# Kernel optimization log

Measured on AMD Instinct MI355X. Metric: run time of the kernel, lower is better.

## Reference

```python
import jax, jax.numpy as jnp
import numpy as np

DIM = 128
N_NODES = 100000     # total semantic-network nodes per graph
N_EDGES = 800000
META0 = 20000        # output_dim0: offset of author block in graph 0
META1 = 20000        # output_dim1
AUTHOR_NUM = 50000   # args.author_num
B = 8192             # batch (chunked into B/2 pairs)
OUT_DIM = 2          # output_dim


def _linear_params(k, out_d, in_d):
    kw, kb = jax.random.split(k)
    s = 1.0 / np.sqrt(in_d)
    W = jax.random.uniform(kw, (out_d, in_d), minval=-s, maxval=s, dtype=jnp.float32)
    b = jax.random.uniform(kb, (out_d,), minval=-s, maxval=s, dtype=jnp.float32)
    return W, b


def setup_inputs() -> dict:
    key = jax.random.key(0)
    ks = jax.random.split(key, 24)
    inp = {
        'semantic_embedding0': jax.random.normal(ks[0], (N_NODES, DIM), jnp.float32),
        'interval0': jax.random.uniform(ks[1], (N_EDGES,), jnp.float32),
        'edge_index0': jax.random.randint(ks[2], (2, N_EDGES), 0, N_NODES, jnp.int64 if jax.config.jax_enable_x64 else jnp.int32),
        'semantic_embedding1': jax.random.normal(ks[3], (N_NODES, DIM), jnp.float32),
        'interval1': jax.random.uniform(ks[4], (N_EDGES,), jnp.float32),
        'edge_index1': jax.random.randint(ks[5], (2, N_EDGES), 0, N_NODES, jnp.int64 if jax.config.jax_enable_x64 else jnp.int32),
        'central_node_emb0': jax.random.normal(ks[6], (B, DIM), jnp.float32),
        'central_node_emb1': jax.random.normal(ks[7], (B, DIM), jnp.float32),
        'data': jax.random.randint(ks[8], (B,), 0, AUTHOR_NUM, jnp.int64 if jax.config.jax_enable_x64 else jnp.int32),
        'structure_embedding': jax.random.normal(ks[9], (B, DIM), jnp.float32),
    }
    inp['W1'], inp['b1'] = _linear_params(ks[10], DIM * 5, DIM)
    inp['W2'], inp['b2'] = _linear_params(ks[11], OUT_DIM, DIM * 5)
    inp['W3'], inp['b3'] = _linear_params(ks[12], DIM, DIM)
    inp['W4'], inp['b4'] = _linear_params(ks[13], DIM, DIM)
    inp['W6'], inp['b6'] = _linear_params(ks[14], DIM, DIM)
    inp['W7'], inp['b7'] = _linear_params(ks[15], DIM, DIM)
    inp['W9'], inp['b9'] = _linear_params(ks[16], DIM, DIM)
    inp['W10'], inp['b10'] = _linear_params(ks[17], DIM, DIM)
    inp['W12'], inp['b12'] = _linear_params(ks[18], DIM, DIM)
    inp['Wc'], inp['bc'] = _linear_params(ks[19], DIM, DIM * 3)
    # Hawkes decay params (nn.Parameter zeros(128,1); small random so decay is nontrivial)
    inp['hp0'] = jax.random.normal(ks[20], (DIM, 1), jnp.float32) * 0.02
    inp['hp1'] = jax.random.normal(ks[21], (DIM, 1), jnp.float32) * 0.02
    return inp


def _hawkes(interval, emb, edge_index, params, meta_size):
    # gather -> exp temporal decay -> scatter-add
    row, col = edge_index[0], edge_index[1]
    theta = (emb @ params)[col]                      # [E, 1]
    x_j = jnp.exp(interval[:, None] * theta) * emb[col]  # [E, D]
    agg = jax.ops.segment_sum(x_j, row, num_segments=N_NODES)  # [N, D]
    return agg[meta_size:meta_size + AUTHOR_NUM]     # [AUTHOR_NUM, D]


def reference(semantic_embedding0, interval0, edge_index0,
              semantic_embedding1, interval1, edge_index1,
              central_node_emb0, central_node_emb1, data, structure_embedding,
              W1, b1, W2, b2, W3, b3, W4, b4, W6, b6, W7, b7,
              W9, b9, W10, b10, W12, b12, Wc, bc, hp0, hp1):
    e0 = semantic_embedding0 @ W3.T + b3
    e1 = semantic_embedding1 @ W4.T + b4
    e0 = jax.nn.relu(_hawkes(interval0, e0, edge_index0, hp0, META0))
    e1 = jax.nn.relu(_hawkes(interval1, e1, edge_index1, hp1, META1))
    e0 = e0[data] @ W6.T + b6
    e1 = e1[data] @ W7.T + b7
    e0 = central_node_emb0 @ W9.T + b9 + e0
    e1 = central_node_emb1 @ W10.T + b10 + e1
    e3 = structure_embedding @ W12.T + b12
    cat = jnp.concatenate([e0, e1, e3], axis=1)      # [B, 3D]
    emb = jax.nn.relu(cat @ Wc.T + bc)               # Concat_Layer
    pre, suf = jnp.split(emb, 2, axis=0)
    emb = jnp.abs(pre - suf)                         # [B/2, D]
    emb = jax.nn.relu(emb @ W1.T + b1)
    # dropout is identity in eval mode
    return emb @ W2.T + b2                           # [B/2, OUT_DIM]
```

## Files before the change

kernel.cpp:

```cpp
#include <hip/hip_runtime.h>
#include <hip/hip_bf16.h>
#include <hip/hip_fp16.h>

typedef _Float16 f16;
typedef __attribute__((ext_vector_type(8))) _Float16 f16x8;
typedef __attribute__((ext_vector_type(4))) float f32x4;

#define N_NODES 100000
#define N_EDGES 800000
#define META 20000
#define AUTHORS 50000
#define BATCH 8192
#define DIM 128
#define CAP 40

__device__ __forceinline__ f16x8 cvtf8(const float* p) {
    float4 x = *(const float4*)p, y = *(const float4*)(p + 4);
    f16x8 a;
    a[0] = (f16)x.x; a[1] = (f16)x.y; a[2] = (f16)x.z; a[3] = (f16)x.w;
    a[4] = (f16)y.x; a[5] = (f16)y.y; a[6] = (f16)y.z; a[7] = (f16)y.w;
    return a;
}

__global__ __launch_bounds__(256) void k_prep_fuse(
    const float* __restrict__ Wc, const float* __restrict__ W9,
    const float* __restrict__ W6, const float* __restrict__ W10,
    const float* __restrict__ W7, const float* __restrict__ W12,
    const float* __restrict__ W3, const float* __restrict__ W4,
    const float* __restrict__ bc, const float* __restrict__ b9,
    const float* __restrict__ b6, const float* __restrict__ b10,
    const float* __restrict__ b7, const float* __restrict__ b12,
    const float* __restrict__ b3, const float* __restrict__ b4,
    const float* __restrict__ hp0, const float* __restrict__ hp1,
    const float* __restrict__ W1, const int* __restrict__ data,
    f16* __restrict__ G, float* __restrict__ biasF, f16* __restrict__ W1F,
    f16* __restrict__ W3F, f16* __restrict__ W4F, float* __restrict__ uc,
    int* __restrict__ needed, int* __restrict__ nneed)
{
    const int blk = blockIdx.x;
    const int tid = threadIdx.x;
    if (blk < 5) {
        __shared__ f16 Wt[128 * 136];
        const float* Wsrc; int co;
        switch (blk) {
            case 0: Wsrc = W9;  co = 0;   break;
            case 1: Wsrc = W6;  co = 0;   break;
            case 2: Wsrc = W10; co = 128; break;
            case 3: Wsrc = W7;  co = 128; break;
            default: Wsrc = W12; co = 256; break;
        }
#pragma unroll 4
        for (int i = 0; i < 64; ++i) {
            const int flat = i * 256 + tid;
            const int k = flat >> 7, t = flat & 127;
            Wt[t * 136 + k] = (f16)Wsrc[flat];
        }
        __syncthreads();
        const int w = tid >> 6, lane = tid & 63;
        const int quad = lane >> 4, l16 = lane & 15;
        f32x4 acc[2][8];
#pragma unroll
        for (int dt = 0; dt < 2; ++dt)
#pragma unroll
            for (int nt = 0; nt < 8; ++nt) acc[dt][nt] = (f32x4)(0.0f);
#pragma unroll
        for (int ks = 0; ks < 4; ++ks) {
            const int k0 = ks * 32 + quad * 8;
#pragma unroll
            for (int dt = 0; dt < 2; ++dt) {
                const int row = w * 32 + dt * 16 + l16;
                f16x8 a = cvtf8(Wc + row * 384 + co + k0);
#pragma unroll
                for (int nt = 0; nt < 8; ++nt) {
                    f16x8 b = *(const f16x8*)&Wt[(nt * 16 + l16) * 136 + k0];
                    acc[dt][nt] = __builtin_amdgcn_mfma_f32_16x16x32_f16(a, b, acc[dt][nt], 0, 0, 0);
                }
            }
        }
#pragma unroll
        for (int dt = 0; dt < 2; ++dt)
#pragma unroll
            for (int nt = 0; nt < 8; ++nt)
#pragma unroll
                for (int r = 0; r < 4; ++r)
                    G[(blk * 128 + w * 32 + dt * 16 + quad * 4 + r) * 128 + nt * 16 + l16] =
                        (f16)acc[dt][nt][r];
    } else if (blk == 5) {
        __shared__ float hpl[256];
        __shared__ float bsum[384];
        hpl[tid] = (tid < 128) ? hp0[tid] : hp1[tid - 128];
        for (int i = tid; i < 384; i += 256) {
            float v;
            if (i < 128) v = b9[i] + b6[i];
            else if (i < 256) v = b10[i - 128] + b7[i - 128];
            else v = b12[i - 256];
            bsum[i] = v;
        }
        __syncthreads();
        {
            const int t = tid & 127;
            const float* W = (tid < 128) ? W3 : W4;
            const float* hh = (tid < 128) ? hpl : hpl + 128;
            float s = 0.f;
#pragma unroll 8
            for (int k = 0; k < 128; ++k) s += W[k * 128 + t] * hh[k];
            uc[(tid < 128 ? 0 : 132) + t] = s;
        }
        if (tid == 0) {
            float s = 0.f;
#pragma unroll 8
            for (int k = 0; k < 128; ++k) s += b3[k] * hpl[k];
            uc[128] = s;
        }
        if (tid == 64) {
            float s = 0.f;
#pragma unroll 8
            for (int k = 0; k < 128; ++k) s += b4[k] * hpl[128 + k];
            uc[132 + 128] = s;
        }
        if (tid < 128) {
            float s = bc[tid];
#pragma unroll 8
            for (int k = 0; k < 384; ++k) s += Wc[tid * 384 + k] * bsum[k];
            biasF[tid] = s;
        }
    } else if (blk < 11) {
        const long base = (long)(blk - 6) * 2048;
#pragma unroll
        for (int i = 0; i < 8; ++i) {
            const long c = base + i * 256 + tid;
            *(f16x8*)(W1F + c * 8) = cvtf8(W1 + c * 8);
        }
    } else if (blk == 11) {
#pragma unroll
        for (int i = 0; i < 8; ++i) {
            const long c = i * 256 + tid;
            *(f16x8*)(W3F + c * 8) = cvtf8(W3 + c * 8);
        }
    } else if (blk == 12) {
#pragma unroll
        for (int i = 0; i < 8; ++i) {
            const long c = i * 256 + tid;
            *(f16x8*)(W4F + c * 8) = cvtf8(W4 + c * 8);
        }
    } else {
        const int i = (blk - 13) * 256 + tid;
        const int a = data[i];
        const int old = atomicCAS(&needed[a], 0, -1);
        if (old == 0) needed[a] = 1 + atomicAdd(nneed, 1);
    }
}

__global__ __launch_bounds__(256) void k_count_emit(
    const int* __restrict__ ei0, const float* __restrict__ iv0,
    const int* __restrict__ ei1, const float* __restrict__ iv1,
    const int* __restrict__ needed,
    int* __restrict__ count, int2* __restrict__ bucket)
{
    const int z = blockIdx.z;
    const int* rows = z ? ei1 : ei0;
    const int* cols = rows + N_EDGES;
    const float* ivp = z ? iv1 : iv0;

    const int e0 = (blockIdx.x * 256 + threadIdx.x) * 4;
    if (e0 >= N_EDGES) return;
    const int4 rr = *(const int4*)(rows + e0);
    const int ra[4] = {rr.x, rr.y, rr.z, rr.w};
#pragma unroll
    for (int j = 0; j < 4; ++j) {
        const int a = ra[j] - META;
        if ((unsigned)a < (unsigned)AUTHORS) {
            const int id = needed[a];
            if (id) {
                const int d = (z << 13) + id - 1;
                const int slot = atomicAdd(&count[d], 1);
                if (slot < CAP) {
                    int2 rec;
                    rec.x = cols[e0 + j];
                    rec.y = __float_as_int(ivp[e0 + j]);
                    bucket[(long)d * CAP + slot] = rec;
                }
            }
        }
    }
}

__global__ __launch_bounds__(512) void k_accum_agg(
    const int* __restrict__ count, const int2* __restrict__ bucket,
    const float* __restrict__ sem0, const float* __restrict__ sem1,
    const float* __restrict__ uc,
    const f16* __restrict__ W3F, const f16* __restrict__ W4F,
    const float* __restrict__ b3, const float* __restrict__ b4,
    f16* __restrict__ aggF)
{
    __shared__ __align__(16) float sld[16][132];
    __shared__ float tl[16];
    const int w = threadIdx.x >> 6, lane = threadIdx.x & 63;
    const int half = lane >> 5, l32 = lane & 31;
    const int gbase = blockIdx.x * 16;
    const int gid = gbase + w * 2 + half;
    const int z = gbase >> 13;
    const float* sem = z ? sem1 : sem0;
    const float* u = uc + (z ? 132 : 0);
    const float cc = u[128];
    const float4 uA = *(const float4*)(u + l32 * 4);

    int n = count[gid];
    n = n < CAP ? n : CAP;
    const long bb = (long)gid * CAP;
    int c1 = 0, c2 = 0; float v1 = 0.f, v2 = 0.f;
    if (l32 < n)      { int2 rec = bucket[bb + l32];      c1 = rec.x; v1 = __int_as_float(rec.y); }
    if (l32 + 32 < n) { int2 rec = bucket[bb + 32 + l32]; c2 = rec.x; v2 = __int_as_float(rec.y); }
    const int nmax = max(n, __shfl_xor(n, 32));

    f32x4 s4 = (f32x4)(0.0f);
    float tt = 0.f;
    for (int e = 0; e < nmax; ++e) {
        const int sl = half * 32 + (e & 31);
        const int ce = __shfl(e < 32 ? c1 : c2, sl);
        const float ve = __shfl(e < 32 ? v1 : v2, sl);
        const float4 r = *(const float4*)(sem + (long)ce * DIM + l32 * 4);
        float p = r.x * uA.x + r.y * uA.y + r.z * uA.z + r.w * uA.w;
        p += __shfl_xor(p, 1);  p += __shfl_xor(p, 2);  p += __shfl_xor(p, 4);
        p += __shfl_xor(p, 8);  p += __shfl_xor(p, 16);
        float d = expf(fminf(ve * (p + cc), 60.f));
        d = (e < n) ? d : 0.f;
        s4[0] += d * r.x; s4[1] += d * r.y; s4[2] += d * r.z; s4[3] += d * r.w;
        tt += d;
    }
    const int lrow = w * 2 + half;
    *(f32x4*)&sld[lrow][l32 * 4] = s4;
    if (l32 == 0) tl[lrow] = tt;
    __syncthreads();

    const int quad = lane >> 4, l16 = lane & 15;
    const f16* WF = z ? W4F : W3F;
    const float* bia = z ? b4 : b3;
    const int cb = w * 16;
    f32x4 acc = (f32x4)(0.0f);
#pragma unroll
    for (int ks = 0; ks < 4; ++ks) {
        const int k0 = ks * 32 + quad * 8;
        f16x8 a = cvtf8(&sld[l16][k0]);
        f16x8 b = *(const f16x8*)(WF + (cb + l16) * DIM + k0);
        acc = __builtin_amdgcn_mfma_f32_16x16x32_f16(a, b, acc, 0, 0, 0);
    }
    const float bcol = bia[cb + l16];
#pragma unroll
    for (int r = 0; r < 4; ++r) {
        const int row = quad * 4 + r;
        const float v = acc[r] + tl[row] * bcol;
        aggF[(long)(gbase + row) * DIM + cb + l16] = (f16)fmaxf(v, 0.f);
    }
}

__global__ __launch_bounds__(512) void k_head_tail(
    const float* __restrict__ cne0, const float* __restrict__ cne1,
    const float* __restrict__ str, const int* __restrict__ data,
    const int* __restrict__ needed, const f16* __restrict__ aggF,
    const f16* __restrict__ G, const float* __restrict__ biasF,
    const f16* __restrict__ W1F, const float* __restrict__ b1,
    const float* __restrict__ W2, const float* __restrict__ b2,
    float* __restrict__ out)
{
    __shared__ __align__(16) float emb[32][132];
    __shared__ float red[8][16][2];
    const int w = threadIdx.x >> 6, lane = threadIdx.x & 63;
    const int quad = lane >> 4, l16 = lane & 15;
    const int pb = blockIdx.x;

    {
        const int rhalf = w >> 2;
        const int cb = (w & 3) * 32;
        const int row = pb * 16 + rhalf * 4096 + l16;
        const int idx = needed[data[row]] - 1;
        f32x4 acc[2];
        acc[0] = (f32x4)(0.0f); acc[1] = (f32x4)(0.0f);
#pragma unroll
        for (int ks = 0; ks < 20; ++ks) {
            const int src = ks >> 2;
            const int k0 = (ks & 3) * 32 + quad * 8;
            f16x8 a;
            if (src == 0 || src == 2 || src == 4) {
                const float* S = (src == 0) ? cne0 : ((src == 2) ? cne1 : str);
                a = cvtf8(S + (long)row * DIM + k0);
            } else {
                a = *(const f16x8*)(aggF + ((src == 1) ? 0L : (8192L * DIM)) + (long)idx * DIM + k0);
            }
            const f16* Gs = G + (long)src * 128 * 128;
#pragma unroll
            for (int nt = 0; nt < 2; ++nt) {
                f16x8 b = *(const f16x8*)(Gs + (cb + nt * 16 + l16) * 128 + k0);
                acc[nt] = __builtin_amdgcn_mfma_f32_16x16x32_f16(a, b, acc[nt], 0, 0, 0);
            }
        }
#pragma unroll
        for (int nt = 0; nt < 2; ++nt) {
            const int col = cb + nt * 16 + l16;
            const float bvv = biasF[col];
#pragma unroll
            for (int r = 0; r < 4; ++r)
                emb[rhalf * 16 + quad * 4 + r][col] = fmaxf(acc[nt][r] + bvv, 0.f);
        }
    }
    __syncthreads();

    const int cbase = w * 80;
    f32x4 acc[5];
#pragma unroll
    for (int t = 0; t < 5; ++t) acc[t] = (f32x4)(0.0f);
#pragma unroll
    for (int ks = 0; ks < 4; ++ks) {
        const int k0 = ks * 32 + quad * 8;
        float4 x1 = *(const float4*)&emb[l16][k0];
        float4 x2 = *(const float4*)&emb[l16][k0 + 4];
        float4 y1 = *(const float4*)&emb[16 + l16][k0];
        float4 y2 = *(const float4*)&emb[16 + l16][k0 + 4];
        f16x8 a;
        a[0] = (f16)fabsf(x1.x - y1.x); a[1] = (f16)fabsf(x1.y - y1.y);
        a[2] = (f16)fabsf(x1.z - y1.z); a[3] = (f16)fabsf(x1.w - y1.w);
        a[4] = (f16)fabsf(x2.x - y2.x); a[5] = (f16)fabsf(x2.y - y2.y);
        a[6] = (f16)fabsf(x2.z - y2.z); a[7] = (f16)fabsf(x2.w - y2.w);
#pragma unroll
        for (int nt = 0; nt < 5; ++nt) {
            f16x8 b = *(const f16x8*)(W1F + (cbase + nt * 16 + l16) * 128 + k0);
            acc[nt] = __builtin_amdgcn_mfma_f32_16x16x32_f16(a, b, acc[nt], 0, 0, 0);
        }
    }
    float p0r[4] = {0.f, 0.f, 0.f, 0.f}, p1r[4] = {0.f, 0.f, 0.f, 0.f};
#pragma unroll
    for (int nt = 0; nt < 5; ++nt) {
        const int col = cbase + nt * 16 + l16;
        const float w20 = W2[col], w21 = W2[640 + col];
        const float bb = b1[col];
#pragma unroll
        for (int r = 0; r < 4; ++r) {
            const float v = fmaxf(acc[nt][r] + bb, 0.f);
            p0r[r] += v * w20;
            p1r[r] += v * w21;
        }
    }
#pragma unroll
    for (int r = 0; r < 4; ++r) {
#pragma unroll
        for (int m = 1; m <= 8; m <<= 1) {
            p0r[r] += __shfl_xor(p0r[r], m);
            p1r[r] += __shfl_xor(p1r[r], m);
        }
    }
    if (l16 == 0) {
#pragma unroll
        for (int r = 0; r < 4; ++r) {
            red[w][quad * 4 + r][0] = p0r[r];
            red[w][quad * 4 + r][1] = p1r[r];
        }
    }
    __syncthreads();
    if (threadIdx.x < 32) {
        const int rr = threadIdx.x >> 1, o = threadIdx.x & 1;
        float s = b2[o];
#pragma unroll
        for (int q = 0; q < 8; ++q) s += red[q][rr][o];
        out[(pb * 16 + rr) * 2 + o] = s;
    }
}

extern "C" void kernel_launch(void* const* d_in, const int* in_sizes, int n_in,
                              void* d_out, int out_size, void* d_ws, size_t ws_size,
                              hipStream_t stream) {
    const float* sem0 = (const float*)d_in[0];
    const float* iv0  = (const float*)d_in[1];
    const int*   ei0  = (const int*)d_in[2];
    const float* sem1 = (const float*)d_in[3];
    const float* iv1  = (const float*)d_in[4];
    const int*   ei1  = (const int*)d_in[5];
    const float* cne0 = (const float*)d_in[6];
    const float* cne1 = (const float*)d_in[7];
    const int*   data = (const int*)d_in[8];
    const float* str  = (const float*)d_in[9];
    const float* W1  = (const float*)d_in[10]; const float* b1  = (const float*)d_in[11];
    const float* W2  = (const float*)d_in[12]; const float* b2  = (const float*)d_in[13];
    const float* W3  = (const float*)d_in[14]; const float* b3  = (const float*)d_in[15];
    const float* W4  = (const float*)d_in[16]; const float* b4  = (const float*)d_in[17];
    const float* W6  = (const float*)d_in[18]; const float* b6  = (const float*)d_in[19];
    const float* W7  = (const float*)d_in[20]; const float* b7  = (const float*)d_in[21];
    const float* W9  = (const float*)d_in[22]; const float* b9  = (const float*)d_in[23];
    const float* W10 = (const float*)d_in[24]; const float* b10 = (const float*)d_in[25];
    const float* W12 = (const float*)d_in[26]; const float* b12 = (const float*)d_in[27];
    const float* Wc  = (const float*)d_in[28]; const float* bc  = (const float*)d_in[29];
    const float* hp0 = (const float*)d_in[30]; const float* hp1 = (const float*)d_in[31];

    char* ws = (char*)d_ws;
    int*    needed = (int*)(ws + 0);
    int*    nneed  = (int*)(ws + 200192);
    int*    count  = (int*)(ws + 200448);
    float*  uc     = (float*)(ws + 266240);
    f16*    W3F    = (f16*)(ws + 267520);
    f16*    W4F    = (f16*)(ws + 300288);
    int2*   bucket = (int2*)(ws + 333056);
    f16*    aggF   = (f16*)(ws + 14030080);
    f16*    G      = (f16*)(ws + 18224384);
    float*  biasF  = (float*)(ws + 18388224);
    f16*    W1F    = (f16*)(ws + 18388736);

    (void)in_sizes; (void)n_in; (void)out_size; (void)ws_size;

    hipMemsetAsync(ws, 0, 265984, stream);
    k_prep_fuse<<<45, 256, 0, stream>>>(Wc, W9, W6, W10, W7, W12, W3, W4,
                                        bc, b9, b6, b10, b7, b12, b3, b4,
                                        hp0, hp1, W1, data,
                                        G, biasF, W1F, W3F, W4F, uc,
                                        needed, nneed);
    k_count_emit<<<dim3(782, 1, 2), 256, 0, stream>>>(ei0, iv0, ei1, iv1,
                                                      needed, count, bucket);
    k_accum_agg<<<1024, 512, 0, stream>>>(count, bucket, sem0, sem1, uc,
                                          W3F, W4F, b3, b4, aggF);
    k_head_tail<<<256, 512, 0, stream>>>(cne0, cne1, str, data, needed, aggF,
                                         G, biasF, W1F, b1, W2, b2,
                                         (float*)d_out);
}
```

Measured before the change: 260.1 us.

## Split id assignment, fuse weight prep with edge emit, unroll accumulate by two

Moves the batch-id dedup into its own small kernel, then merges the weight-preparation blocks with the edge count/emit pass into a single launch so the weight conversions overlap with edge bucketing. The emit path now loads column indices and intervals as vectors up front instead of scattered per-edge loads. The accumulation loop handles two gathered edges per iteration, so both row loads are in flight together and their shuffle reductions interleave, and it uses exp2f with a prescaled argument. The exp rewrite slightly changes rounding, and the kernel count stays the same.

```diff
diff --git a/kernel.cpp b/kernel.cpp
--- a/kernel.cpp
+++ b/kernel.cpp
@@ -22,7 +22,16 @@
     return a;
 }
 
-__global__ __launch_bounds__(256) void k_prep_fuse(
+__global__ __launch_bounds__(256) void k_ids(
+    const int* __restrict__ data, int* __restrict__ needed, int* __restrict__ nneed)
+{
+    const int i = blockIdx.x * 256 + threadIdx.x;
+    const int a = data[i];
+    const int old = atomicCAS(&needed[a], 0, -1);
+    if (old == 0) needed[a] = 1 + atomicAdd(nneed, 1);
+}
+
+__global__ __launch_bounds__(256) void k_emit_prep(
     const float* __restrict__ Wc, const float* __restrict__ W9,
     const float* __restrict__ W6, const float* __restrict__ W10,
     const float* __restrict__ W7, const float* __restrict__ W12,
@@ -32,10 +41,13 @@
     const float* __restrict__ b7, const float* __restrict__ b12,
     const float* __restrict__ b3, const float* __restrict__ b4,
     const float* __restrict__ hp0, const float* __restrict__ hp1,
-    const float* __restrict__ W1, const int* __restrict__ data,
+    const float* __restrict__ W1,
+    const int* __restrict__ ei0, const float* __restrict__ iv0,
+    const int* __restrict__ ei1, const float* __restrict__ iv1,
+    const int* __restrict__ needed,
     f16* __restrict__ G, float* __restrict__ biasF, f16* __restrict__ W1F,
     f16* __restrict__ W3F, f16* __restrict__ W4F, float* __restrict__ uc,
-    int* __restrict__ needed, int* __restrict__ nneed)
+    int* __restrict__ count, int2* __restrict__ bucket)
 {
     const int blk = blockIdx.x;
     const int tid = threadIdx.x;
@@ -144,41 +156,34 @@
             *(f16x8*)(W4F + c * 8) = cvtf8(W4 + c * 8);
         }
     } else {
-        const int i = (blk - 13) * 256 + tid;
-        const int a = data[i];
-        const int old = atomicCAS(&needed[a], 0, -1);
-        if (old == 0) needed[a] = 1 + atomicAdd(nneed, 1);
-    }
-}
-
-__global__ __launch_bounds__(256) void k_count_emit(
-    const int* __restrict__ ei0, const float* __restrict__ iv0,
-    const int* __restrict__ ei1, const float* __restrict__ iv1,
-    const int* __restrict__ needed,
-    int* __restrict__ count, int2* __restrict__ bucket)
-{
-    const int z = blockIdx.z;
-    const int* rows = z ? ei1 : ei0;
-    const int* cols = rows + N_EDGES;
-    const float* ivp = z ? iv1 : iv0;
-
-    const int e0 = (blockIdx.x * 256 + threadIdx.x) * 4;
-    if (e0 >= N_EDGES) return;
-    const int4 rr = *(const int4*)(rows + e0);
-    const int ra[4] = {rr.x, rr.y, rr.z, rr.w};
-#pragma unroll
-    for (int j = 0; j < 4; ++j) {
-        const int a = ra[j] - META;
-        if ((unsigned)a < (unsigned)AUTHORS) {
-            const int id = needed[a];
-            if (id) {
-                const int d = (z << 13) + id - 1;
-                const int slot = atomicAdd(&count[d], 1);
-                if (slot < CAP) {
-                    int2 rec;
-                    rec.x = cols[e0 + j];
-                    rec.y = __float_as_int(ivp[e0 + j]);
-                    bucket[(long)d * CAP + slot] = rec;
+        const int b = blk - 13;
+        const int z = b / 782;
+        const int xb = b - z * 782;
+        const int e0 = (xb * 256 + tid) * 4;
+        if (e0 >= N_EDGES) return;
+        const int* rows = z ? ei1 : ei0;
+        const int* cols = rows + N_EDGES;
+        const float* ivp = z ? iv1 : iv0;
+        const int4 rr = *(const int4*)(rows + e0);
+        const int4 cc4 = *(const int4*)(cols + e0);
+        const float4 vv4 = *(const float4*)(ivp + e0);
+        const int ra[4] = {rr.x, rr.y, rr.z, rr.w};
+        const int ca[4] = {cc4.x, cc4.y, cc4.z, cc4.w};
+        const float va[4] = {vv4.x, vv4.y, vv4.z, vv4.w};
+#pragma unroll
+        for (int j = 0; j < 4; ++j) {
+            const int a = ra[j] - META;
+            if ((unsigned)a < (unsigned)AUTHORS) {
+                const int id = needed[a];
+                if (id) {
+                    const int d = (z << 13) + id - 1;
+                    const int slot = atomicAdd(&count[d], 1);
+                    if (slot < CAP) {
+                        int2 rec;
+                        rec.x = ca[j];
+                        rec.y = __float_as_int(va[j]);
+                        bucket[(long)d * CAP + slot] = rec;
+                    }
                 }
             }
         }
@@ -215,18 +220,30 @@
 
     f32x4 s4 = (f32x4)(0.0f);
     float tt = 0.f;
-    for (int e = 0; e < nmax; ++e) {
-        const int sl = half * 32 + (e & 31);
-        const int ce = __shfl(e < 32 ? c1 : c2, sl);
-        const float ve = __shfl(e < 32 ? v1 : v2, sl);
-        const float4 r = *(const float4*)(sem + (long)ce * DIM + l32 * 4);
-        float p = r.x * uA.x + r.y * uA.y + r.z * uA.z + r.w * uA.w;
-        p += __shfl_xor(p, 1);  p += __shfl_xor(p, 2);  p += __shfl_xor(p, 4);
-        p += __shfl_xor(p, 8);  p += __shfl_xor(p, 16);
-        float d = expf(fminf(ve * (p + cc), 60.f));
-        d = (e < n) ? d : 0.f;
-        s4[0] += d * r.x; s4[1] += d * r.y; s4[2] += d * r.z; s4[3] += d * r.w;
-        tt += d;
+    for (int e = 0; e < nmax; e += 2) {
+        const int f = e + 1;
+        const int ce0 = __shfl(e < 32 ? c1 : c2, half * 32 + (e & 31));
+        const float ve0 = __shfl(e < 32 ? v1 : v2, half * 32 + (e & 31));
+        const int ce1 = __shfl(f < 32 ? c1 : c2, half * 32 + (f & 31));
+        const float ve1 = __shfl(f < 32 ? v1 : v2, half * 32 + (f & 31));
+        const float4 r0 = *(const float4*)(sem + (long)ce0 * DIM + l32 * 4);
+        const float4 r1 = *(const float4*)(sem + (long)ce1 * DIM + l32 * 4);
+        float p0 = r0.x * uA.x + r0.y * uA.y + r0.z * uA.z + r0.w * uA.w;
+        float p1 = r1.x * uA.x + r1.y * uA.y + r1.z * uA.z + r1.w * uA.w;
+        p0 += __shfl_xor(p0, 1);  p1 += __shfl_xor(p1, 1);
+        p0 += __shfl_xor(p0, 2);  p1 += __shfl_xor(p1, 2);
+        p0 += __shfl_xor(p0, 4);  p1 += __shfl_xor(p1, 4);
+        p0 += __shfl_xor(p0, 8);  p1 += __shfl_xor(p1, 8);
+        p0 += __shfl_xor(p0, 16); p1 += __shfl_xor(p1, 16);
+        float d0 = exp2f(fminf(ve0 * (p0 + cc) * 1.44269504089f, 86.562f));
+        float d1 = exp2f(fminf(ve1 * (p1 + cc) * 1.44269504089f, 86.562f));
+        d0 = (e < n) ? d0 : 0.f;
+        d1 = (f < n) ? d1 : 0.f;
+        s4[0] += d0 * r0.x + d1 * r1.x;
+        s4[1] += d0 * r0.y + d1 * r1.y;
+        s4[2] += d0 * r0.z + d1 * r1.z;
+        s4[3] += d0 * r0.w + d1 * r1.w;
+        tt += d0 + d1;
     }
     const int lrow = w * 2 + half;
     *(f32x4*)&sld[lrow][l32 * 4] = s4;
@@ -406,13 +423,13 @@
     (void)in_sizes; (void)n_in; (void)out_size; (void)ws_size;
 
     hipMemsetAsync(ws, 0, 265984, stream);
-    k_prep_fuse<<<45, 256, 0, stream>>>(Wc, W9, W6, W10, W7, W12, W3, W4,
-                                        bc, b9, b6, b10, b7, b12, b3, b4,
-                                        hp0, hp1, W1, data,
-                                        G, biasF, W1F, W3F, W4F, uc,
-                                        needed, nneed);
-    k_count_emit<<<dim3(782, 1, 2), 256, 0, stream>>>(ei0, iv0, ei1, iv1,
-                                                      needed, count, bucket);
+    k_ids<<<32, 256, 0, stream>>>(data, needed, nneed);
+    k_emit_prep<<<13 + 782 * 2, 256, 0, stream>>>(Wc, W9, W6, W10, W7, W12, W3, W4,
+                                                  bc, b9, b6, b10, b7, b12, b3, b4,
+                                                  hp0, hp1, W1,
+                                                  ei0, iv0, ei1, iv1, needed,
+                                                  G, biasF, W1F, W3F, W4F, uc,
+                                                  count, bucket);
     k_accum_agg<<<1024, 512, 0, stream>>>(count, bucket, sem0, sem1, uc,
                                           W3F, W4F, b3, b4, aggF);
     k_head_tail<<<256, 512, 0, stream>>>(cne0, cne1, str, data, needed, aggF,
```

New measurement: 248.5 us. 1.05x faster.
